# Kernel optimization log

Measured on AMD Instinct MI355X. Metric: run time of the kernel, lower is better.

The kernel has to match this reference:

```python
import jax, jax.numpy as jnp
import numpy as np

N_FFT = 400          # Whisper n_fft
HOP = 160            # Whisper hop_length
CUT = N_FFT // 2 + 1 # freq_cutoff = 201
T_SIG = 9_600_000    # 10 minutes @ 16 kHz


def _make_basis():
    # fourier_basis[k, n] = exp(-2*pi*i*k*n/N); keep first CUT rows,
    # stack [real; imag], multiply by periodic Hann window.
    n = jnp.arange(N_FFT, dtype=jnp.float32)
    k = jnp.arange(CUT, dtype=jnp.float32)
    ang = (2.0 * jnp.pi / N_FFT) * k[:, None] * n[None, :]          # [CUT, N_FFT]
    window = 0.5 * (1.0 - jnp.cos(2.0 * jnp.pi * n / N_FFT))        # periodic Hann
    basis = jnp.concatenate([jnp.cos(ang), -jnp.sin(ang)], axis=0)  # [2*CUT, N_FFT]
    return (basis * window[None, :]).astype(jnp.float32)


def setup_inputs() -> dict:
    key = jax.random.key(0)
    signal = jax.random.normal(key, (T_SIG,), dtype=jnp.float32)
    basis = _make_basis()  # conv weight, exact DFT basis (frozen in original)
    return {"signal": signal, "basis": basis}


def reference(signal, basis):
    # zero-pad by freq_cutoff-1 on each side, then strided conv == windowed DFT
    pad = CUT - 1
    x = jnp.pad(signal, (pad, pad))[None, None, :]          # [1, 1, T+2*pad]
    w = basis[:, None, :]                                    # [2*CUT, 1, N_FFT]
    y = jax.lax.conv_general_dilated(
        x, w, window_strides=(HOP,), padding='VALID',
        dimension_numbers=('NCH', 'OIH', 'NCH'))             # [1, 2*CUT, frames]
    real = y[:, :CUT, :]
    imag = y[:, CUT:2 * CUT, :]
    return real, imag
```

## Files before the change

kernel.cpp:

```cpp
#include <hip/hip_runtime.h>

#define HOP 160
#define NROWS 402
#define NTAPS 400
#define T_SIG 9600000
#define N_FRAMES 60001
#define PAD 200

#define MT 13
#define KS 26
#define FPB 128
#define MGROUPS 4
#define NBT ((N_FRAMES + FPB - 1) / FPB)
#define SPAN (127*HOP + 416)
#define SPAN4 (SPAN/4)
#define LDSE 21776

typedef __bf16 bf16x8 __attribute__((ext_vector_type(8)));
typedef float f32x16 __attribute__((ext_vector_type(16)));
typedef unsigned short u16x8 __attribute__((ext_vector_type(8)));
typedef unsigned short u16x4 __attribute__((ext_vector_type(4)));

__device__ __forceinline__ unsigned short f2bf(float f) {
    unsigned int u = __builtin_bit_cast(unsigned int, f);
    u += 0x7fffu + ((u >> 16) & 1u);
    return (unsigned short)(u >> 16);
}

__global__ void stft_prep(const float* __restrict__ basis,
                          unsigned short* __restrict__ packed) {
    int tid = blockIdx.x * 256 + threadIdx.x;
    if (tid >= MT * KS * 64) return;
    int lane = tid & 63;
    int frag = tid >> 6;
    int ks = frag % KS;
    int mt = frag / KS;
    int row = mt * 32 + (lane & 31);
    int colb = ks * 16 + (lane >> 5) * 8;
    u16x8 v;
#pragma unroll
    for (int i = 0; i < 8; ++i) {
        int col = colb + i;
        float f = (row < NROWS && col < NTAPS) ? basis[row * NTAPS + col] : 0.0f;
        v[i] = f2bf(f);
    }
    *reinterpret_cast<u16x8*>(packed + (size_t)tid * 8) = v;
}

__launch_bounds__(256, 3)
__global__ void stft_mfma(const float* __restrict__ sig,
                          const unsigned short* __restrict__ packedA,
                          float* __restrict__ out) {
    __shared__ unsigned short sl[LDSE];
    const int tid = threadIdx.x;
    const int bg = blockIdx.x & (MGROUPS - 1);
    const int bt = blockIdx.x >> 2;
    const int lane = tid & 63;
    const int w = tid >> 6;
    const int mt = bg * 4 + w;

    bf16x8 afr[KS];
    if (mt < MT) {
        const unsigned short* pA = packedA + ((size_t)(mt * KS) * 64 + lane) * 8;
#pragma unroll
        for (int ks = 0; ks < KS; ++ks)
            afr[ks] = *reinterpret_cast<const bf16x8*>(pA + (size_t)ks * 512);
    }

    const long sbase = (long)bt * (FPB * HOP) - PAD;
    for (int idx = tid; idx < SPAN4; idx += 256) {
        const int e = idx * 4;
        const long g0 = sbase + e;
        float4 v;
        if (g0 >= 0 && g0 + 4 <= (long)T_SIG) {
            v = *reinterpret_cast<const float4*>(sig + g0);
        } else {
            v.x = (g0 + 0 >= 0 && g0 + 0 < (long)T_SIG) ? sig[g0 + 0] : 0.0f;
            v.y = (g0 + 1 >= 0 && g0 + 1 < (long)T_SIG) ? sig[g0 + 1] : 0.0f;
            v.z = (g0 + 2 >= 0 && g0 + 2 < (long)T_SIG) ? sig[g0 + 2] : 0.0f;
            v.w = (g0 + 3 >= 0 && g0 + 3 < (long)T_SIG) ? sig[g0 + 3] : 0.0f;
        }
        u16x4 s;
        s[0] = f2bf(v.x); s[1] = f2bf(v.y); s[2] = f2bf(v.z); s[3] = f2bf(v.w);
        const int pos = e + 8 * (e / 160);
        *reinterpret_cast<u16x4*>(&sl[pos]) = s;
    }
    __syncthreads();

    if (mt >= MT) return;

    const int l31 = lane & 31;
    const int g = lane >> 5;
    const int rb = mt * 32 + 4 * g;

#pragma unroll 1
    for (int i = 0; i < FPB / 32; ++i) {
        const int lf = i * 32 + l31;
        const long t = (long)bt * FPB + lf;
        const unsigned short* bb = &sl[lf * 168 + g * 8];
        f32x16 acc = {0,0,0,0,0,0,0,0,0,0,0,0,0,0,0,0};
#pragma unroll
        for (int ks = 0; ks < KS; ++ks) {
            const bf16x8 b = *reinterpret_cast<const bf16x8*>(bb + ks * 16 + 8 * (ks / 10));
            acc = __builtin_amdgcn_mfma_f32_32x32x16_bf16(afr[ks], b, acc, 0, 0, 0);
        }
        if (t < N_FRAMES) {
#pragma unroll
            for (int r = 0; r < 16; ++r) {
                const int row = rb + (r & 3) + 8 * (r >> 2);
                if (row < NROWS) out[(long)row * N_FRAMES + t] = acc[r];
            }
        }
    }
}

__global__ void stft_naive(const float* __restrict__ sig,
                           const float* __restrict__ basis,
                           float* __restrict__ out) {
    long idx = (long)blockIdx.x * 256 + threadIdx.x;
    if (idx >= (long)NROWS * N_FRAMES) return;
    int row = (int)(idx / N_FRAMES);
    int tt = (int)(idx % N_FRAMES);
    long s0 = (long)tt * HOP - PAD;
    float acc = 0.0f;
    for (int n = 0; n < NTAPS; ++n) {
        long s = s0 + n;
        float x = (s >= 0 && s < (long)T_SIG) ? sig[s] : 0.0f;
        acc = fmaf(x, basis[row * NTAPS + n], acc);
    }
    out[idx] = acc;
}

extern "C" void kernel_launch(void* const* d_in, const int* in_sizes, int n_in,
                              void* d_out, int out_size, void* d_ws, size_t ws_size,
                              hipStream_t stream) {
    (void)in_sizes; (void)n_in; (void)out_size;
    const float* sig = (const float*)d_in[0];
    const float* basis = (const float*)d_in[1];
    float* out = (float*)d_out;
    const size_t need = (size_t)MT * KS * 64 * 8 * sizeof(unsigned short);
    if (ws_size >= need) {
        unsigned short* packed = (unsigned short*)d_ws;
        stft_prep<<<(MT * KS * 64 + 255) / 256, 256, 0, stream>>>(basis, packed);
        stft_mfma<<<NBT * MGROUPS, 256, 0, stream>>>(sig, packed, out);
    } else {
        long total = (long)NROWS * N_FRAMES;
        stft_naive<<<(int)((total + 255) / 256), 256, 0, stream>>>(sig, basis, out);
    }
}
```

Before: 69.24 us.

## Use four independent accumulators and issue A-fragment loads via inline asm

The serial loop over four 32-frame subtiles becomes a single fully unrolled K loop. Each A fragment now feeds four independent MFMA chains, one per subtile, which exposes more instruction-level parallelism and hides MFMA dependency latency. The A fragments are fetched with inline-asm global loads issued before the signal staging, with an explicit vmcnt wait afterwards, so those loads overlap the LDS fill. The cost is higher register pressure from four f32x16 accumulators plus 26 A fragments, so launch bounds drop to 2 blocks per CU.

```diff
diff --git a/kernel.cpp b/kernel.cpp
--- a/kernel.cpp
+++ b/kernel.cpp
@@ -10,16 +10,16 @@
 #define MT 13
 #define KS 26
 #define FPB 128
-#define MGROUPS 4
-#define NBT ((N_FRAMES + FPB - 1) / FPB)
-#define SPAN (127*HOP + 416)
-#define SPAN4 (SPAN/4)
+#define NBT 469
+#define SPAN4 5184
 #define LDSE 21776
+#define NEED1 346112UL
 
 typedef __bf16 bf16x8 __attribute__((ext_vector_type(8)));
 typedef float f32x16 __attribute__((ext_vector_type(16)));
 typedef unsigned short u16x8 __attribute__((ext_vector_type(8)));
 typedef unsigned short u16x4 __attribute__((ext_vector_type(4)));
+typedef unsigned int u32x4 __attribute__((ext_vector_type(4)));
 
 __device__ __forceinline__ unsigned short f2bf(float f) {
     unsigned int u = __builtin_bit_cast(unsigned int, f);
@@ -27,8 +27,8 @@
     return (unsigned short)(u >> 16);
 }
 
-__global__ void stft_prep(const float* __restrict__ basis,
-                          unsigned short* __restrict__ packed) {
+__global__ void prep_a(const float* __restrict__ basis,
+                       unsigned short* __restrict__ packed) {
     int tid = blockIdx.x * 256 + threadIdx.x;
     if (tid >= MT * KS * 64) return;
     int lane = tid & 63;
@@ -47,24 +47,33 @@
     *reinterpret_cast<u16x8*>(packed + (size_t)tid * 8) = v;
 }
 
-__launch_bounds__(256, 3)
-__global__ void stft_mfma(const float* __restrict__ sig,
-                          const unsigned short* __restrict__ packedA,
+#define STORE_ACC(A, R0, T) do { if ((T) < (long)N_FRAMES) { _Pragma("unroll") \
+    for (int r = 0; r < 16; ++r) { \
+        int row = (R0) + (r & 3) + 8 * (r >> 2); \
+        if (row < NROWS) out[(long)row * N_FRAMES + (T)] = (A)[r]; \
+    } } } while (0)
+
+__launch_bounds__(256, 2)
+__global__ void stft_areg(const float* __restrict__ sig,
+                          const unsigned short* __restrict__ apack,
                           float* __restrict__ out) {
     __shared__ unsigned short sl[LDSE];
     const int tid = threadIdx.x;
-    const int bg = blockIdx.x & (MGROUPS - 1);
+    const int bm = blockIdx.x & 3;
     const int bt = blockIdx.x >> 2;
     const int lane = tid & 63;
     const int w = tid >> 6;
-    const int mt = bg * 4 + w;
+    const int mt = bm * 4 + w;
 
-    bf16x8 afr[KS];
+    u32x4 a4[KS];
     if (mt < MT) {
-        const unsigned short* pA = packedA + ((size_t)(mt * KS) * 64 + lane) * 8;
+        const char* ab = (const char*)apack + ((size_t)(mt * KS) * 64 + lane) * 16;
 #pragma unroll
-        for (int ks = 0; ks < KS; ++ks)
-            afr[ks] = *reinterpret_cast<const bf16x8*>(pA + (size_t)ks * 512);
+        for (int ks = 0; ks < KS; ++ks) {
+            asm volatile("global_load_dwordx4 %0, %1, off"
+                         : "=v"(a4[ks])
+                         : "v"(ab + (size_t)ks * 1024));
+        }
     }
 
     const long sbase = (long)bt * (FPB * HOP) - PAD;
@@ -80,38 +89,46 @@
             v.z = (g0 + 2 >= 0 && g0 + 2 < (long)T_SIG) ? sig[g0 + 2] : 0.0f;
             v.w = (g0 + 3 >= 0 && g0 + 3 < (long)T_SIG) ? sig[g0 + 3] : 0.0f;
         }
-        u16x4 s;
-        s[0] = f2bf(v.x); s[1] = f2bf(v.y); s[2] = f2bf(v.z); s[3] = f2bf(v.w);
+        u16x4 s4;
+        s4[0] = f2bf(v.x); s4[1] = f2bf(v.y); s4[2] = f2bf(v.z); s4[3] = f2bf(v.w);
         const int pos = e + 8 * (e / 160);
-        *reinterpret_cast<u16x4*>(&sl[pos]) = s;
+        *reinterpret_cast<u16x4*>(&sl[pos]) = s4;
     }
     __syncthreads();
+    asm volatile("s_waitcnt vmcnt(0)" ::: "memory");
+    __builtin_amdgcn_sched_barrier(0);
 
     if (mt >= MT) return;
 
     const int l31 = lane & 31;
     const int g = lane >> 5;
+    const char* bBase = (const char*)sl + l31 * 336 + g * 16;
+
+    f32x16 acc0 = {0,0,0,0,0,0,0,0,0,0,0,0,0,0,0,0};
+    f32x16 acc1 = {0,0,0,0,0,0,0,0,0,0,0,0,0,0,0,0};
+    f32x16 acc2 = {0,0,0,0,0,0,0,0,0,0,0,0,0,0,0,0};
+    f32x16 acc3 = {0,0,0,0,0,0,0,0,0,0,0,0,0,0,0,0};
+
+#pragma unroll
+    for (int ka = 0; ka < KS; ++ka) {
+        const int sc = ka * 32 + (ka >= 10 ? 16 : 0) + (ka >= 20 ? 16 : 0);
+        const bf16x8 a = __builtin_bit_cast(bf16x8, a4[ka]);
+        bf16x8 b0 = *reinterpret_cast<const bf16x8*>(bBase + sc);
+        bf16x8 b1 = *reinterpret_cast<const bf16x8*>(bBase + 10752 + sc);
+        bf16x8 b2 = *reinterpret_cast<const bf16x8*>(bBase + 21504 + sc);
+        bf16x8 b3 = *reinterpret_cast<const bf16x8*>(bBase + 32256 + sc);
+        acc0 = __builtin_amdgcn_mfma_f32_32x32x16_bf16(a, b0, acc0, 0, 0, 0);
+        acc1 = __builtin_amdgcn_mfma_f32_32x32x16_bf16(a, b1, acc1, 0, 0, 0);
+        acc2 = __builtin_amdgcn_mfma_f32_32x32x16_bf16(a, b2, acc2, 0, 0, 0);
+        acc3 = __builtin_amdgcn_mfma_f32_32x32x16_bf16(a, b3, acc3, 0, 0, 0);
+    }
+
     const int rb = mt * 32 + 4 * g;
-
-#pragma unroll 1
-    for (int i = 0; i < FPB / 32; ++i) {
-        const int lf = i * 32 + l31;
-        const long t = (long)bt * FPB + lf;
-        const unsigned short* bb = &sl[lf * 168 + g * 8];
-        f32x16 acc = {0,0,0,0,0,0,0,0,0,0,0,0,0,0,0,0};
-#pragma unroll
-        for (int ks = 0; ks < KS; ++ks) {
-            const bf16x8 b = *reinterpret_cast<const bf16x8*>(bb + ks * 16 + 8 * (ks / 10));
-            acc = __builtin_amdgcn_mfma_f32_32x32x16_bf16(afr[ks], b, acc, 0, 0, 0);
-        }
-        if (t < N_FRAMES) {
-#pragma unroll
-            for (int r = 0; r < 16; ++r) {
-                const int row = rb + (r & 3) + 8 * (r >> 2);
-                if (row < NROWS) out[(long)row * N_FRAMES + t] = acc[r];
-            }
-        }
-    }
+    const long tb = (long)bt * FPB + l31;
+    STORE_ACC(acc0, rb, tb);
+    STORE_ACC(acc1, rb, tb + 32);
+    STORE_ACC(acc2, rb, tb + 64);
+    STORE_ACC(acc3, rb, tb + 96);
 }
 
 __global__ void stft_naive(const float* __restrict__ sig,
@@ -138,11 +155,10 @@
     const float* sig = (const float*)d_in[0];
     const float* basis = (const float*)d_in[1];
     float* out = (float*)d_out;
-    const size_t need = (size_t)MT * KS * 64 * 8 * sizeof(unsigned short);
-    if (ws_size >= need) {
-        unsigned short* packed = (unsigned short*)d_ws;
-        stft_prep<<<(MT * KS * 64 + 255) / 256, 256, 0, stream>>>(basis, packed);
-        stft_mfma<<<NBT * MGROUPS, 256, 0, stream>>>(sig, packed, out);
+    if (ws_size >= NEED1) {
+        unsigned short* ap = (unsigned short*)d_ws;
+        prep_a<<<(MT * KS * 64 + 255) / 256, 256, 0, stream>>>(basis, ap);
+        stft_areg<<<NBT * 4, 256, 0, stream>>>(sig, ap, out);
     } else {
         long total = (long)NROWS * N_FRAMES;
         stft_naive<<<(int)((total + 255) / 256), 256, 0, stream>>>(sig, basis, out);
```

Result: slower. 78.17 us (+12.9%).
